# Optimization experiments

Hardware: AMD Instinct MI355X
Metric: run time of the kernel (lower is better)

## Reference

```python
import jax, jax.numpy as jnp
import numpy as np

ATTN_SPLITS = 2
TEMPERATURE = 10000.0

# ---------- split / merge helpers (faithful to split_feature / merge_splits) ----------

def split_cf(x, ns):  # channel-first [b,c,h,w] -> [b*ns*ns, c, h/ns, w/ns]
    b, c, h, w = x.shape
    x = x.reshape(b, c, ns, h // ns, ns, w // ns).transpose(0, 2, 4, 1, 3, 5)
    return x.reshape(b * ns * ns, c, h // ns, w // ns)

def merge_cf(x, ns):  # channel-first inverse
    b, c, h, w = x.shape
    nb = b // (ns * ns)
    x = x.reshape(nb, ns, ns, c, h, w).transpose(0, 3, 1, 4, 2, 5)
    return x.reshape(nb, c, ns * h, ns * w)

def split_cl(x, ns):  # channel-last [b,h,w,c] -> [b*ns*ns, h/ns, w/ns, c]
    b, h, w, c = x.shape
    x = x.reshape(b, ns, h // ns, ns, w // ns, c).transpose(0, 1, 3, 2, 4, 5)
    return x.reshape(b * ns * ns, h // ns, w // ns, c)

def merge_cl(x, ns):  # channel-last inverse
    b, h, w, c = x.shape
    nb = b // (ns * ns)
    x = x.reshape(nb, ns, ns, h, w, c).transpose(0, 1, 3, 2, 4, 5)
    return x.reshape(nb, ns * h, ns * w, c)

# ---------- PositionEmbeddingSine (normalize=True, scale=2*pi) ----------

def pos_embed_sine(h, w, num_pos_feats):
    scale = 2.0 * np.pi
    eps = 1e-6
    ones = jnp.ones((h, w), jnp.float32)
    y_embed = jnp.cumsum(ones, 0)
    x_embed = jnp.cumsum(ones, 1)
    y_embed = y_embed / (y_embed[-1:, :] + eps) * scale
    x_embed = x_embed / (x_embed[:, -1:] + eps) * scale
    dim_t = jnp.arange(num_pos_feats, dtype=jnp.float32)
    dim_t = TEMPERATURE ** (2.0 * jnp.floor(dim_t / 2.0) / num_pos_feats)
    pos_x = x_embed[:, :, None] / dim_t  # [h,w,npf]
    pos_y = y_embed[:, :, None] / dim_t
    pos_x = jnp.stack([jnp.sin(pos_x[:, :, 0::2]), jnp.cos(pos_x[:, :, 1::2])], -1).reshape(h, w, -1)
    pos_y = jnp.stack([jnp.sin(pos_y[:, :, 0::2]), jnp.cos(pos_y[:, :, 1::2])], -1).reshape(h, w, -1)
    pos = jnp.concatenate([pos_y, pos_x], -1)  # [h,w,c]
    return jnp.transpose(pos, (2, 0, 1))[None]  # [1,c,h,w]

def feature_add_position(f0, f1, attn_splits, c):
    if attn_splits > 1:
        f0s = split_cf(f0, attn_splits)
        f1s = split_cf(f1, attn_splits)
        pos = pos_embed_sine(f0s.shape[2], f0s.shape[3], c // 2)
        return merge_cf(f0s + pos, attn_splits), merge_cf(f1s + pos, attn_splits)
    pos = pos_embed_sine(f0.shape[2], f0.shape[3], c // 2)
    return f0 + pos, f1 + pos

# ---------- shifted-window attention mask (static, numpy) ----------

def shift_window_attn_mask(h, w, ns):
    wsh, wsw = h // ns, w // ns
    ssh, ssw = wsh // 2, wsw // 2
    img = np.zeros((h, w), np.float32)
    cnt = 0
    for hs in (slice(0, -wsh), slice(-wsh, -ssh), slice(-ssh, None)):
        for ws in (slice(0, -wsw), slice(-wsw, -ssw), slice(-ssw, None)):
            img[hs, ws] = cnt
            cnt += 1
    m = img.reshape(ns, wsh, ns, wsw).transpose(0, 2, 1, 3).reshape(ns * ns, wsh * wsw)
    am = m[:, None, :] - m[:, :, None]
    am = np.where(am != 0, -100.0, 0.0).astype(np.float32)
    return jnp.asarray(am)  # [ns*ns, N, N]

# ---------- single-head split (shifted) window attention ----------

def split_window_attention(q, k, v, ns, h, w, attn_mask):
    b, _, c = q.shape
    bn = b * ns * ns
    wsh, wsw = h // ns, w // ns
    ssh, ssw = wsh // 2, wsw // 2
    q = q.reshape(b, h, w, c)
    k = k.reshape(b, h, w, c)
    v = v.reshape(b, h, w, c)
    q = jnp.roll(q, (-ssh, -ssw), (1, 2))
    k = jnp.roll(k, (-ssh, -ssw), (1, 2))
    v = jnp.roll(v, (-ssh, -ssw), (1, 2))
    qs = split_cl(q, ns).reshape(bn, -1, c)
    ks = split_cl(k, ns).reshape(bn, -1, c)
    vs = split_cl(v, ns).reshape(bn, -1, c)
    scores = jnp.einsum('bnc,bmc->bnm', qs, ks) / jnp.sqrt(jnp.asarray(c, qs.dtype))
    scores = scores + jnp.tile(attn_mask, (b, 1, 1))
    attn = jax.nn.softmax(scores, axis=-1)
    out = jnp.einsum('bnm,bmc->bnc', attn, vs)
    out = merge_cl(out.reshape(bn, wsh, wsw, c), ns)
    out = jnp.roll(out, (ssh, ssw), (1, 2))
    return out.reshape(b, -1, c)

# ---------- global correlation softmax matching ----------

def global_correlation_softmax(f0, f1):
    b, c, h, w = f0.shape
    f0v = f0.reshape(b, c, -1)  # [b,c,hw]
    f1v = f1.reshape(b, c, -1)
    corr = jnp.einsum('bcn,bcm->bnm', f0v, f1v) / jnp.sqrt(jnp.asarray(c, f0.dtype))
    yy, xx = jnp.meshgrid(jnp.arange(h), jnp.arange(w), indexing='ij')
    grid = jnp.stack([xx, yy], 0).astype(f0.dtype)  # [2,h,w] (x,y)
    gridv = grid.reshape(2, -1).T  # [hw,2]
    prob = jax.nn.softmax(corr, axis=-1)
    corresp = jnp.einsum('bnm,md->bnd', prob, gridv).reshape(b, h, w, 2).transpose(0, 3, 1, 2)
    flow = corresp - grid[None]
    return flow

# ---------- setup & reference ----------

def setup_inputs() -> dict:
    key = jax.random.key(0)
    k0, k1 = jax.random.split(key)
    b, c, h, w = 4, 128, 64, 64
    feature0 = jax.random.normal(k0, (b, c, h, w), jnp.float32)
    feature1 = jax.random.normal(k1, (b, c, h, w), jnp.float32)
    return {'feature0': feature0, 'feature1': feature1}

def reference(feature0, feature1):
    b, c, h, w = feature0.shape
    ns = ATTN_SPLITS
    f0, f1 = feature_add_position(feature0, feature1, ns, c)
    attn_mask = shift_window_attn_mask(h, w, ns)
    q = f0.reshape(b, c, -1).transpose(0, 2, 1)  # [b,hw,c]
    kv = f1.reshape(b, c, -1).transpose(0, 2, 1)
    f0_attn = split_window_attention(q, kv, kv, ns, h, w, attn_mask)  # [b,hw,c]
    f0_attn = f0_attn.transpose(0, 2, 1).reshape(b, c, h, w)
    flow = global_correlation_softmax(f0_attn, f1)  # [b,2,h,w]
    return flow
```

## Files before the change

kernel.cpp:

```cpp
#include <hip/hip_runtime.h>
#include <hip/hip_bf16.h>
#include <math.h>

#define NB 4
#define NC 128
#define NH 64
#define NW 64
#define NHW 4096
#define SCALE 0.08838834764831845f

typedef short bf16x8 __attribute__((ext_vector_type(8)));
typedef float f32x4 __attribute__((ext_vector_type(4)));

__device__ __forceinline__ unsigned bfbits(float f) {
    unsigned u = __float_as_uint(f);
    return (u + 0x7FFFu + ((u >> 16) & 1u)) >> 16;
}
__device__ __forceinline__ unsigned bfpair(float a, float b) {
    return bfbits(a) | (bfbits(b) << 16);
}

__global__ __launch_bounds__(256) void pos_kernel(float* __restrict__ pos) {
    int idx = blockIdx.x * 256 + threadIdx.x;
    if (idx >= NC * 32 * 32) return;
    int x = idx & 31;
    int y = (idx >> 5) & 31;
    int c = idx >> 10;
    const float twopi = 6.283185307179586f;
    const float denom = 32.0f + 1e-6f;
    int cc = (c < 64) ? c : (c - 64);
    float e = (c < 64) ? (float)(y + 1) : (float)(x + 1);
    e = e * (twopi / denom);
    int k = cc >> 1;
    float arg = e * exp2f(-0.41524101186091903f * (float)k);
    pos[idx] = (cc & 1) ? cosf(arg) : sinf(arg);
}

__global__ __launch_bounds__(256) void pack_kernel(
        const float* __restrict__ f0, const float* __restrict__ f1,
        const float* __restrict__ pos,
        __hip_bfloat16* __restrict__ F0t, __hip_bfloat16* __restrict__ Bt,
        __hip_bfloat16* __restrict__ Ktw) {
    __shared__ float T[64][129];
    int blk = blockIdx.x;
    const bool isA = blk < 256;
    const float* src = isA ? f0 : f1;
    blk &= 255;
    const int y = blk & 63;
    const int b = blk >> 6;
    const int tid = threadIdx.x;
    const float* s = src + (size_t)b * NC * NHW + y * 64;
    const float sA = isA ? SCALE : 1.0f;
    for (int idx = tid; idx < 64 * NC; idx += 256) {
        const int x = idx & 63, c = idx >> 6;
        T[x][c] = (s[c * NHW + x] + pos[(c << 10) + ((y & 31) << 5) + (x & 31)]) * sA;
    }
    __syncthreads();
    __hip_bfloat16* dst = isA ? F0t : Bt;
    for (int idx = tid; idx < 512; idx += 256) {
        const int x = idx >> 3, c0 = (idx & 7) * 16;
        const float* tr = &T[x][c0];
        uint4 v0, v1;
        v0.x = bfpair(tr[0], tr[1]);   v0.y = bfpair(tr[2], tr[3]);
        v0.z = bfpair(tr[4], tr[5]);   v0.w = bfpair(tr[6], tr[7]);
        v1.x = bfpair(tr[8], tr[9]);   v1.y = bfpair(tr[10], tr[11]);
        v1.z = bfpair(tr[12], tr[13]); v1.w = bfpair(tr[14], tr[15]);
        __hip_bfloat16* row = dst + ((size_t)b * NHW + y * 64 + x) * NC + c0;
        *reinterpret_cast<uint4*>(row) = v0;
        *reinterpret_cast<uint4*>(row + 8) = v1;
    }
    if (!isA) {
        const int yp = (y + 48) & 63;
        const int wi = yp >> 5, ry = yp & 31;
        const int c = tid >> 1;
        const int wj = tid & 1;
        const int win = b * 4 + wi * 2 + wj;
        unsigned up[16];
        #pragma unroll
        for (int pr = 0; pr < 16; ++pr) {
            const int x0 = ((wj << 5) + 2 * pr + 16) & 63;
            up[pr] = bfpair(T[x0][c], T[x0 + 1][c]);
        }
        __hip_bfloat16* krow = Ktw + ((size_t)win * NC + c) * 1024 + ry * 32;
        uint4* uv = reinterpret_cast<uint4*>(up);
        #pragma unroll
        for (int i = 0; i < 4; ++i)
            *reinterpret_cast<uint4*>(krow + i * 8) = uv[i];
    }
}

__global__ __launch_bounds__(256) void attn_mfma_kernel(
        const __hip_bfloat16* __restrict__ F0t,
        const __hip_bfloat16* __restrict__ Bt,
        const __hip_bfloat16* __restrict__ Ktw,
        __hip_bfloat16* __restrict__ At) {
    __shared__ __align__(16) char lds[73728];
    char* KsB = lds;
    char* VsB = lds + 32768;
    char* Pscr = lds + 65536;
    const int tid = threadIdx.x;
    const int lane = tid & 63;
    const int w = tid >> 6;
    const int l15 = lane & 15;
    const int g = lane >> 4;
    const int blk = blockIdx.x;
    const int win = blk >> 4;
    const int qt = blk & 15;
    const int b = win >> 2, wi = (win >> 1) & 1, wj = win & 1;

    const char* Btb = (const char*)(Bt + (size_t)b * NHW * NC);
    const char* Vsrc = (const char*)(Ktw + (size_t)win * NC * 1024);

    bf16x8 qf[4];
    {
        const int tok = qt * 64 + w * 16 + l15;
        const int yo = ((wi << 5) + (tok >> 5) + 16) & 63;
        const int xo = ((wj << 5) + (tok & 31) + 16) & 63;
        const __hip_bfloat16* qrow =
            F0t + ((size_t)b * NHW + yo * 64 + xo) * NC + g * 8;
        #pragma unroll
        for (int kk = 0; kk < 4; ++kk)
            qf[kk] = *reinterpret_cast<const bf16x8*>(qrow + kk * 32);
    }

    const int reg_q = (wi ? (qt < 8 ? 1 : 2) : 0) * 3
                    + (wj ? ((w & 1) == 0 ? 1 : 2) : 0);

    auto stageK = [&](int buf, int kt) {
        char* dst = KsB + buf * 16384;
        #pragma unroll
        for (int it = 0; it < 4; ++it) {
            const int obase = w * 4096 + it * 1024;
            const int row = w * 16 + it * 4 + (lane >> 4);
            const int tok = kt * 64 + row;
            const int yo = ((wi << 5) + (tok >> 5) + 16) & 63;
            const int xo = ((wj << 5) + (tok & 31) + 16) & 63;
            const char* src = Btb + (yo * 64 + xo) * 256 +
                              (((lane & 15) * 16) ^ ((row & 7) << 4));
            __builtin_amdgcn_global_load_lds(
                (const __attribute__((address_space(1))) void*)src,
                (__attribute__((address_space(3))) void*)(dst + obase), 16, 0, 0);
        }
    };
    auto stageV = [&](int buf, int kt) {
        char* dst = VsB + buf * 16384;
        #pragma unroll
        for (int it = 0; it < 4; ++it) {
            const int obase = w * 4096 + it * 1024;
            const int o = obase + lane * 16;
            const int crow = o >> 7;
            const int off = o & 127;
            __builtin_amdgcn_global_load_lds(
                (const __attribute__((address_space(1))) void*)(Vsrc + crow * 2048 + kt * 128 + (off ^ ((crow & 7) << 4))),
                (__attribute__((address_space(3))) void*)(dst + obase), 16, 0, 0);
        }
    };

    f32x4 oacc[8] = {{0,0,0,0},{0,0,0,0},{0,0,0,0},{0,0,0,0},
                     {0,0,0,0},{0,0,0,0},{0,0,0,0},{0,0,0,0}};
    float zacc = 0.f;

    stageK(0, 0); stageV(0, 0);
    __syncthreads();

    for (int kt = 0; kt < 16; ++kt) {
        const int buf = kt & 1;
        if (kt < 15) { stageK(buf ^ 1, kt + 1); stageV(buf ^ 1, kt + 1); }

        const char* kb = KsB + buf * 16384;
        f32x4 sacc[4] = {{0,0,0,0},{0,0,0,0},{0,0,0,0},{0,0,0,0}};
        #pragma unroll
        for (int kk = 0; kk < 4; ++kk) {
            #pragma unroll
            for (int msub = 0; msub < 4; ++msub) {
                const int byte = msub * 4096 + l15 * 256 + ((kk * 64 + g * 16) ^ ((l15 & 7) << 4));
                bf16x8 kf = *reinterpret_cast<const bf16x8*>(kb + byte);
                sacc[msub] = __builtin_amdgcn_mfma_f32_16x16x32_bf16(kf, qf[kk], sacc[msub], 0, 0, 0);
            }
        }

        const int rk_row = (wi ? (kt < 8 ? 1 : 2) : 0) * 3;
        char* pw = Pscr + w * 2048;
        #pragma unroll
        for (int msub = 0; msub < 4; ++msub) {
            const int rk = rk_row + (wj ? ((msub & 1) == 0 ? 1 : 2) : 0);
            const bool ok = (rk == reg_q);
            const float p0 = ok ? __expf(sacc[msub][0]) : 0.f;
            const float p1 = ok ? __expf(sacc[msub][1]) : 0.f;
            const float p2 = ok ? __expf(sacc[msub][2]) : 0.f;
            const float p3 = ok ? __expf(sacc[msub][3]) : 0.f;
            zacc += (p0 + p1) + (p2 + p3);
            *reinterpret_cast<unsigned*>(pw + l15 * 128 + ((msub * 32 + g * 8 + 0) ^ ((l15 & 7) << 4))) = bfpair(p0, p1);
            *reinterpret_cast<unsigned*>(pw + l15 * 128 + ((msub * 32 + g * 8 + 4) ^ ((l15 & 7) << 4))) = bfpair(p2, p3);
        }
        bf16x8 pf[2];
        #pragma unroll
        for (int kk = 0; kk < 2; ++kk)
            pf[kk] = *reinterpret_cast<const bf16x8*>(pw + l15 * 128 + ((kk * 64 + g * 16) ^ ((l15 & 7) << 4)));

        const char* vb = VsB + buf * 16384;
        #pragma unroll
        for (int kk = 0; kk < 2; ++kk) {
            #pragma unroll
            for (int co = 0; co < 8; ++co) {
                const int byte = (co * 16 + l15) * 128 + ((kk * 64 + g * 16) ^ ((l15 & 7) << 4));
                bf16x8 vf = *reinterpret_cast<const bf16x8*>(vb + byte);
                oacc[co] = __builtin_amdgcn_mfma_f32_16x16x32_bf16(pf[kk], vf, oacc[co], 0, 0, 0);
            }
        }
        __syncthreads();
    }

    float z = zacc;
    z += __shfl_xor(z, 16);
    z += __shfl_xor(z, 32);

    unsigned short* olds = reinterpret_cast<unsigned short*>(lds + w * 4096);
    #pragma unroll
    for (int r = 0; r < 4; ++r) {
        const float zi = SCALE / __shfl(z, g * 4 + r);
        #pragma unroll
        for (int co = 0; co < 8; ++co)
            olds[(g * 4 + r) * 128 + co * 16 + l15] = (unsigned short)bfbits(oacc[co][r] * zi);
    }

    const int qloc = lane >> 2;
    const int c0 = (lane & 3) * 32;
    const int tok = qt * 64 + w * 16 + qloc;
    const int yo = ((wi << 5) + (tok >> 5) + 16) & 63;
    const int xo = ((wj << 5) + (tok & 31) + 16) & 63;
    __hip_bfloat16* arow = At + ((size_t)b * NHW + yo * 64 + xo) * NC + c0;
    #pragma unroll
    for (int i = 0; i < 4; ++i) {
        int4 v = *reinterpret_cast<const int4*>(olds + qloc * 128 + c0 + i * 8);
        *reinterpret_cast<int4*>(arow + i * 8) = v;
    }
}

__global__ __launch_bounds__(256, 2) void corr_part_kernel(
        const __hip_bfloat16* __restrict__ At,
        const __hip_bfloat16* __restrict__ Bt,
        float4* __restrict__ part) {
    __shared__ __hip_bfloat16 Bs[2][64 * 128];
    const int tid = threadIdx.x;
    const int lane = tid & 63;
    const int w = tid >> 6;
    const int blk = blockIdx.x;
    const int ms = blk & 7;
    const int nt = (blk >> 3) & 15;
    const int b = blk >> 7;
    const int l15 = lane & 15;
    const int g = lane >> 4;
    const int n0 = nt * 256 + w * 64;

    const __hip_bfloat16* Ab = At + (size_t)b * NHW * NC;
    const __hip_bfloat16* Bb = Bt + (size_t)b * NHW * NC;

    bf16x8 afrag[4][4];
    #pragma unroll
    for (int s = 0; s < 4; ++s) {
        const __hip_bfloat16* arow = Ab + (size_t)(n0 + s * 16 + l15) * NC + g * 8;
        #pragma unroll
        for (int kk = 0; kk < 4; ++kk)
            afrag[s][kk] = *reinterpret_cast<const bf16x8*>(arow + kk * 32);
    }

    auto stage = [&](int buf, int mtile) {
        const char* srcbase = reinterpret_cast<const char*>(Bb + (size_t)mtile * 64 * NC);
        #pragma unroll
        for (int it = 0; it < 4; ++it) {
            const int obase = w * 4096 + it * 1024;
            const int o = obase + lane * 16;
            const int row = o >> 8;
            const int off = o & 255;
            const char* src = srcbase + row * 256 + (off ^ ((row & 7) << 4));
            __builtin_amdgcn_global_load_lds(
                (const __attribute__((address_space(1))) void*)src,
                (__attribute__((address_space(3))) void*)((char*)&Bs[buf][0] + obase),
                16, 0, 0);
        }
    };

    f32x4 rl[4]  = {{0,0,0,0},{0,0,0,0},{0,0,0,0},{0,0,0,0}};
    f32x4 rsm[4] = {{0,0,0,0},{0,0,0,0},{0,0,0,0},{0,0,0,0}};
    f32x4 rsy[4] = {{0,0,0,0},{0,0,0,0},{0,0,0,0},{0,0,0,0}};

    stage(0, ms * 8);
    __syncthreads();

    for (int mt = 0; mt < 8; ++mt) {
        const int buf = mt & 1;
        if (mt < 7) stage(buf ^ 1, ms * 8 + mt + 1);

        f32x4 acc[4][4] = {{{0,0,0,0},{0,0,0,0},{0,0,0,0},{0,0,0,0}},
                           {{0,0,0,0},{0,0,0,0},{0,0,0,0},{0,0,0,0}},
                           {{0,0,0,0},{0,0,0,0},{0,0,0,0},{0,0,0,0}},
                           {{0,0,0,0},{0,0,0,0},{0,0,0,0},{0,0,0,0}}};
        const char* base = (const char*)&Bs[buf][0];
        #pragma unroll
        for (int kk = 0; kk < 4; ++kk) {
            #pragma unroll
            for (int msub = 0; msub < 4; ++msub) {
                const int byte = msub * 4096 + l15 * 256 +
                                 ((kk * 64 + g * 16) ^ ((l15 & 7) << 4));
                bf16x8 bfrag = *reinterpret_cast<const bf16x8*>(base + byte);
                #pragma unroll
                for (int s = 0; s < 4; ++s)
                    acc[s][msub] = __builtin_amdgcn_mfma_f32_16x16x32_bf16(
                        afrag[s][kk], bfrag, acc[s][msub], 0, 0, 0);
            }
        }
        const float y0 = (float)(ms * 8 + mt);
        #pragma unroll
        for (int s = 0; s < 4; ++s) {
            #pragma unroll
            for (int r = 0; r < 4; ++r) {
                float p0 = __expf(acc[s][0][r]);
                float p1 = __expf(acc[s][1][r]);
                float p2 = __expf(acc[s][2][r]);
                float p3 = __expf(acc[s][3][r]);
                float ts = (p0 + p1) + (p2 + p3);
                rl[s][r]  += ts;
                rsy[s][r] += y0 * ts;
                rsm[s][r] += fmaf(3.f, p3, fmaf(2.f, p2, p1));
            }
        }
        __syncthreads();
    }

    const float xl = (float)l15;
    #pragma unroll
    for (int s = 0; s < 4; ++s) {
        #pragma unroll
        for (int r = 0; r < 4; ++r) {
            float a  = rl[s][r];
            float sx = xl * rl[s][r] + 16.f * rsm[s][r];
            float sy = rsy[s][r];
            #pragma unroll
            for (int m = 1; m < 16; m <<= 1) {
                a  += __shfl_xor(a, m);
                sx += __shfl_xor(sx, m);
                sy += __shfl_xor(sy, m);
            }
            if (l15 == 0) {
                const int n = n0 + s * 16 + g * 4 + r;
                part[((size_t)b * NHW + n) * 8 + ms] = make_float4(a, sx, sy, 0.f);
            }
        }
    }
}

__global__ __launch_bounds__(256) void finalize_kernel(
        const float4* __restrict__ part, float* __restrict__ out) {
    const int idx = blockIdx.x * 256 + threadIdx.x;
    if (idx >= NB * NHW) return;
    const int n = idx & (NHW - 1);
    const int b = idx >> 12;
    float l = 0.f, sx = 0.f, sy = 0.f;
    #pragma unroll
    for (int i = 0; i < 8; ++i) {
        float4 p = part[(size_t)idx * 8 + i];
        l += p.x; sx += p.y; sy += p.z;
    }
    const float inv = 1.0f / l;
    out[(size_t)b * 2 * NHW + n]       = sx * inv - (float)(n & 63);
    out[(size_t)b * 2 * NHW + NHW + n] = sy * inv - (float)(n >> 6);
}

extern "C" void kernel_launch(void* const* d_in, const int* in_sizes, int n_in,
                              void* d_out, int out_size, void* d_ws, size_t ws_size,
                              hipStream_t stream) {
    const float* f0 = (const float*)d_in[0];
    const float* f1 = (const float*)d_in[1];
    float* pos = (float*)d_ws;
    __hip_bfloat16* F0t = (__hip_bfloat16*)(pos + 131072);
    __hip_bfloat16* Bt  = F0t + (size_t)NB * NHW * NC;
    __hip_bfloat16* Ktw = Bt  + (size_t)NB * NHW * NC;
    __hip_bfloat16* At  = Ktw + (size_t)16 * NC * 1024;
    float4* part = (float4*)(At + (size_t)NB * NHW * NC);
    float* out = (float*)d_out;

    pos_kernel<<<512, 256, 0, stream>>>(pos);
    pack_kernel<<<512, 256, 0, stream>>>(f0, f1, pos, F0t, Bt, Ktw);
    attn_mfma_kernel<<<256, 256, 0, stream>>>(F0t, Bt, Ktw, At);
    corr_part_kernel<<<512, 256, 0, stream>>>(At, Bt, part);
    finalize_kernel<<<64, 256, 0, stream>>>(part, out);
}
```

Measured before the change: 70.96 us.

## Split attention key range across wave pairs and read V directly from global

The attention kernel now runs 512 blocks of 32 queries instead of 256 blocks of 64. Wave pairs split the key tiles into even and odd halves and merge their partial outputs and normalizers through LDS at the end. V is no longer staged in LDS and is read straight from global memory. The query scale now folds in log2(e), so both attention and correlation use exp2f, and the attention output is rescaled by the same factor. The kernel also adds launch_bounds occupancy 2, aiming for more parallelism on 256 CUs, at the cost of uncached-in-LDS V reads and an extra reduction step.

```diff
diff --git a/kernel.cpp b/kernel.cpp
--- a/kernel.cpp
+++ b/kernel.cpp
@@ -8,6 +8,7 @@
 #define NW 64
 #define NHW 4096
 #define SCALE 0.08838834764831845f
+#define PSL2E 0.12753102543365835f
 
 typedef short bf16x8 __attribute__((ext_vector_type(8)));
 typedef float f32x4 __attribute__((ext_vector_type(4)));
@@ -50,7 +51,7 @@
     const int b = blk >> 6;
     const int tid = threadIdx.x;
     const float* s = src + (size_t)b * NC * NHW + y * 64;
-    const float sA = isA ? SCALE : 1.0f;
+    const float sA = isA ? PSL2E : 1.0f;
     for (int idx = tid; idx < 64 * NC; idx += 256) {
         const int x = idx & 63, c = idx >> 6;
         T[x][c] = (s[c * NHW + x] + pos[(c << 10) + ((y & 31) << 5) + (x & 31)]) * sA;
@@ -89,23 +90,23 @@
     }
 }
 
-__global__ __launch_bounds__(256) void attn_mfma_kernel(
+__global__ __launch_bounds__(256, 2) void attn_mfma_kernel(
         const __hip_bfloat16* __restrict__ F0t,
         const __hip_bfloat16* __restrict__ Bt,
         const __hip_bfloat16* __restrict__ Ktw,
         __hip_bfloat16* __restrict__ At) {
     __shared__ __align__(16) char lds[73728];
-    char* KsB = lds;
-    char* VsB = lds + 32768;
     char* Pscr = lds + 65536;
     const int tid = threadIdx.x;
     const int lane = tid & 63;
     const int w = tid >> 6;
+    const int p = w & 1;
+    const int qh = w >> 1;
     const int l15 = lane & 15;
     const int g = lane >> 4;
     const int blk = blockIdx.x;
-    const int win = blk >> 4;
-    const int qt = blk & 15;
+    const int win = blk >> 5;
+    const int qt32 = blk & 31;
     const int b = win >> 2, wi = (win >> 1) & 1, wj = win & 1;
 
     const char* Btb = (const char*)(Bt + (size_t)b * NHW * NC);
@@ -113,7 +114,7 @@
 
     bf16x8 qf[4];
     {
-        const int tok = qt * 64 + w * 16 + l15;
+        const int tok = qt32 * 32 + qh * 16 + l15;
         const int yo = ((wi << 5) + (tok >> 5) + 16) & 63;
         const int xo = ((wj << 5) + (tok & 31) + 16) & 63;
         const __hip_bfloat16* qrow =
@@ -123,16 +124,16 @@
             qf[kk] = *reinterpret_cast<const bf16x8*>(qrow + kk * 32);
     }
 
-    const int reg_q = (wi ? (qt < 8 ? 1 : 2) : 0) * 3
-                    + (wj ? ((w & 1) == 0 ? 1 : 2) : 0);
-
-    auto stageK = [&](int buf, int kt) {
-        char* dst = KsB + buf * 16384;
+    const int reg_q = (wi ? (qt32 < 16 ? 1 : 2) : 0) * 3
+                    + (wj ? (qh == 0 ? 1 : 2) : 0);
+
+    auto stageK = [&](int slot, int ktg) {
+        char* dst = lds + slot * 16384;
         #pragma unroll
         for (int it = 0; it < 4; ++it) {
             const int obase = w * 4096 + it * 1024;
             const int row = w * 16 + it * 4 + (lane >> 4);
-            const int tok = kt * 64 + row;
+            const int tok = ktg * 64 + row;
             const int yo = ((wi << 5) + (tok >> 5) + 16) & 63;
             const int xo = ((wj << 5) + (tok & 31) + 16) & 63;
             const char* src = Btb + (yo * 64 + xo) * 256 +
@@ -142,32 +143,20 @@
                 (__attribute__((address_space(3))) void*)(dst + obase), 16, 0, 0);
         }
     };
-    auto stageV = [&](int buf, int kt) {
-        char* dst = VsB + buf * 16384;
-        #pragma unroll
-        for (int it = 0; it < 4; ++it) {
-            const int obase = w * 4096 + it * 1024;
-            const int o = obase + lane * 16;
-            const int crow = o >> 7;
-            const int off = o & 127;
-            __builtin_amdgcn_global_load_lds(
-                (const __attribute__((address_space(1))) void*)(Vsrc + crow * 2048 + kt * 128 + (off ^ ((crow & 7) << 4))),
-                (__attribute__((address_space(3))) void*)(dst + obase), 16, 0, 0);
-        }
-    };
 
     f32x4 oacc[8] = {{0,0,0,0},{0,0,0,0},{0,0,0,0},{0,0,0,0},
                      {0,0,0,0},{0,0,0,0},{0,0,0,0},{0,0,0,0}};
     float zacc = 0.f;
 
-    stageK(0, 0); stageV(0, 0);
+    stageK(0, 0); stageK(1, 1);
     __syncthreads();
 
-    for (int kt = 0; kt < 16; ++kt) {
-        const int buf = kt & 1;
-        if (kt < 15) { stageK(buf ^ 1, kt + 1); stageV(buf ^ 1, kt + 1); }
-
-        const char* kb = KsB + buf * 16384;
+    int d = 0;
+    for (int s = 0; s < 8; ++s) {
+        const int ktg = 2 * s + p;
+        if (s < 7) { stageK((d ^ 1) * 2 + 0, 2 * s + 2); stageK((d ^ 1) * 2 + 1, 2 * s + 3); }
+
+        const char* kb = lds + (d * 2 + p) * 16384;
         f32x4 sacc[4] = {{0,0,0,0},{0,0,0,0},{0,0,0,0},{0,0,0,0}};
         #pragma unroll
         for (int kk = 0; kk < 4; ++kk) {
@@ -179,16 +168,16 @@
             }
         }
 
-        const int rk_row = (wi ? (kt < 8 ? 1 : 2) : 0) * 3;
+        const int rk_row = (wi ? (ktg < 8 ? 1 : 2) : 0) * 3;
         char* pw = Pscr + w * 2048;
         #pragma unroll
         for (int msub = 0; msub < 4; ++msub) {
             const int rk = rk_row + (wj ? ((msub & 1) == 0 ? 1 : 2) : 0);
             const bool ok = (rk == reg_q);
-            const float p0 = ok ? __expf(sacc[msub][0]) : 0.f;
-            const float p1 = ok ? __expf(sacc[msub][1]) : 0.f;
-            const float p2 = ok ? __expf(sacc[msub][2]) : 0.f;
-            const float p3 = ok ? __expf(sacc[msub][3]) : 0.f;
+            const float p0 = ok ? exp2f(sacc[msub][0]) : 0.f;
+            const float p1 = ok ? exp2f(sacc[msub][1]) : 0.f;
+            const float p2 = ok ? exp2f(sacc[msub][2]) : 0.f;
+            const float p3 = ok ? exp2f(sacc[msub][3]) : 0.f;
             zacc += (p0 + p1) + (p2 + p3);
             *reinterpret_cast<unsigned*>(pw + l15 * 128 + ((msub * 32 + g * 8 + 0) ^ ((l15 & 7) << 4))) = bfpair(p0, p1);
             *reinterpret_cast<unsigned*>(pw + l15 * 128 + ((msub * 32 + g * 8 + 4) ^ ((l15 & 7) << 4))) = bfpair(p2, p3);
@@ -198,42 +187,61 @@
         for (int kk = 0; kk < 2; ++kk)
             pf[kk] = *reinterpret_cast<const bf16x8*>(pw + l15 * 128 + ((kk * 64 + g * 16) ^ ((l15 & 7) << 4)));
 
-        const char* vb = VsB + buf * 16384;
-        #pragma unroll
-        for (int kk = 0; kk < 2; ++kk) {
+        #pragma unroll
+        for (int kk2 = 0; kk2 < 2; ++kk2) {
+            const int tok0 = ktg * 64 + kk2 * 32 + g * 8;
             #pragma unroll
             for (int co = 0; co < 8; ++co) {
-                const int byte = (co * 16 + l15) * 128 + ((kk * 64 + g * 16) ^ ((l15 & 7) << 4));
-                bf16x8 vf = *reinterpret_cast<const bf16x8*>(vb + byte);
-                oacc[co] = __builtin_amdgcn_mfma_f32_16x16x32_bf16(pf[kk], vf, oacc[co], 0, 0, 0);
+                const int c = co * 16 + l15;
+                bf16x8 vf = *reinterpret_cast<const bf16x8*>(
+                    Vsrc + ((size_t)c * 1024 + tok0) * 2);
+                oacc[co] = __builtin_amdgcn_mfma_f32_16x16x32_bf16(pf[kk2], vf, oacc[co], 0, 0, 0);
             }
         }
         __syncthreads();
+        d ^= 1;
     }
 
     float z = zacc;
     z += __shfl_xor(z, 16);
     z += __shfl_xor(z, 32);
 
-    unsigned short* olds = reinterpret_cast<unsigned short*>(lds + w * 4096);
-    #pragma unroll
-    for (int r = 0; r < 4; ++r) {
-        const float zi = SCALE / __shfl(z, g * 4 + r);
-        #pragma unroll
-        for (int co = 0; co < 8; ++co)
-            olds[(g * 4 + r) * 128 + co * 16 + l15] = (unsigned short)bfbits(oacc[co][r] * zi);
-    }
-
-    const int qloc = lane >> 2;
-    const int c0 = (lane & 3) * 32;
-    const int tok = qt * 64 + w * 16 + qloc;
-    const int yo = ((wi << 5) + (tok >> 5) + 16) & 63;
-    const int xo = ((wj << 5) + (tok & 31) + 16) & 63;
-    __hip_bfloat16* arow = At + ((size_t)b * NHW + yo * 64 + xo) * NC + c0;
-    #pragma unroll
-    for (int i = 0; i < 4; ++i) {
-        int4 v = *reinterpret_cast<const int4*>(olds + qloc * 128 + c0 + i * 8);
-        *reinterpret_cast<int4*>(arow + i * 8) = v;
+    float* zl = (float*)(lds + 16384);
+    if (p == 1) {
+        float* od = (float*)(lds + qh * 8192);
+        #pragma unroll
+        for (int r = 0; r < 4; ++r) {
+            #pragma unroll
+            for (int co = 0; co < 8; ++co)
+                od[(g * 4 + r) * 128 + co * 16 + l15] = oacc[co][r];
+        }
+        if (lane < 16) zl[qh * 16 + lane] = z;
+    }
+    __syncthreads();
+    if (p == 0) {
+        const float* od = (const float*)(lds + qh * 8192);
+        const float zc = z + zl[qh * 16 + l15];
+        unsigned short* olds = (unsigned short*)(lds + 16896 + qh * 4096);
+        #pragma unroll
+        for (int r = 0; r < 4; ++r) {
+            const float zi = PSL2E / __shfl(zc, g * 4 + r);
+            #pragma unroll
+            for (int co = 0; co < 8; ++co) {
+                const float o = oacc[co][r] + od[(g * 4 + r) * 128 + co * 16 + l15];
+                olds[(g * 4 + r) * 128 + co * 16 + l15] = (unsigned short)bfbits(o * zi);
+            }
+        }
+        const int qloc = lane >> 2;
+        const int c0 = (lane & 3) * 32;
+        const int tok = qt32 * 32 + qh * 16 + qloc;
+        const int yo = ((wi << 5) + (tok >> 5) + 16) & 63;
+        const int xo = ((wj << 5) + (tok & 31) + 16) & 63;
+        __hip_bfloat16* arow = At + ((size_t)b * NHW + yo * 64 + xo) * NC + c0;
+        #pragma unroll
+        for (int i = 0; i < 4; ++i) {
+            int4 v = *reinterpret_cast<const int4*>(olds + qloc * 128 + c0 + i * 8);
+            *reinterpret_cast<int4*>(arow + i * 8) = v;
+        }
     }
 }
 
@@ -315,10 +323,10 @@
         for (int s = 0; s < 4; ++s) {
             #pragma unroll
             for (int r = 0; r < 4; ++r) {
-                float p0 = __expf(acc[s][0][r]);
-                float p1 = __expf(acc[s][1][r]);
-                float p2 = __expf(acc[s][2][r]);
-                float p3 = __expf(acc[s][3][r]);
+                float p0 = exp2f(acc[s][0][r]);
+                float p1 = exp2f(acc[s][1][r]);
+                float p2 = exp2f(acc[s][2][r]);
+                float p3 = exp2f(acc[s][3][r]);
                 float ts = (p0 + p1) + (p2 + p3);
                 rl[s][r]  += ts;
                 rsy[s][r] += y0 * ts;
@@ -382,7 +390,7 @@
 
     pos_kernel<<<512, 256, 0, stream>>>(pos);
     pack_kernel<<<512, 256, 0, stream>>>(f0, f1, pos, F0t, Bt, Ktw);
-    attn_mfma_kernel<<<256, 256, 0, stream>>>(F0t, Bt, Ktw, At);
+    attn_mfma_kernel<<<512, 256, 0, stream>>>(F0t, Bt, Ktw, At);
     corr_part_kernel<<<512, 256, 0, stream>>>(At, Bt, part);
     finalize_kernel<<<64, 256, 0, stream>>>(part, out);
 }
```

Result: slower. 99.28 us (+39.9%).

## Fold log2e into the scale for exp2f, and retile the correlation kernel finer

Applied to the files above, without the earlier changes.

The attention scale is multiplied by log2(e) in the packed queries and in the attention output normalisation. Both softmax stages can then call exp2f directly instead of __expf, which drops a multiply per exponential. The correlation-partial kernel is retiled: each block now covers 128 query rows and 4 key tiles instead of 256 and 8. That takes the grid from 512 to 2048 blocks and drops the two-blocks-per-CU launch bound, to raise parallelism and reduce register pressure. In exchange, each B tile is re-staged by more blocks, and the partial buffer and the finalize reduction double to 16 slices, which assumes the workspace has room for them.

```diff
diff --git a/kernel.cpp b/kernel.cpp
--- a/kernel.cpp
+++ b/kernel.cpp
@@ -8,6 +8,7 @@
 #define NW 64
 #define NHW 4096
 #define SCALE 0.08838834764831845f
+#define PSL2E 0.12753102543365835f
 
 typedef short bf16x8 __attribute__((ext_vector_type(8)));
 typedef float f32x4 __attribute__((ext_vector_type(4)));
@@ -50,7 +51,7 @@
     const int b = blk >> 6;
     const int tid = threadIdx.x;
     const float* s = src + (size_t)b * NC * NHW + y * 64;
-    const float sA = isA ? SCALE : 1.0f;
+    const float sA = isA ? PSL2E : 1.0f;
     for (int idx = tid; idx < 64 * NC; idx += 256) {
         const int x = idx & 63, c = idx >> 6;
         T[x][c] = (s[c * NHW + x] + pos[(c << 10) + ((y & 31) << 5) + (x & 31)]) * sA;
@@ -185,10 +186,10 @@
         for (int msub = 0; msub < 4; ++msub) {
             const int rk = rk_row + (wj ? ((msub & 1) == 0 ? 1 : 2) : 0);
             const bool ok = (rk == reg_q);
-            const float p0 = ok ? __expf(sacc[msub][0]) : 0.f;
-            const float p1 = ok ? __expf(sacc[msub][1]) : 0.f;
-            const float p2 = ok ? __expf(sacc[msub][2]) : 0.f;
-            const float p3 = ok ? __expf(sacc[msub][3]) : 0.f;
+            const float p0 = ok ? exp2f(sacc[msub][0]) : 0.f;
+            const float p1 = ok ? exp2f(sacc[msub][1]) : 0.f;
+            const float p2 = ok ? exp2f(sacc[msub][2]) : 0.f;
+            const float p3 = ok ? exp2f(sacc[msub][3]) : 0.f;
             zacc += (p0 + p1) + (p2 + p3);
             *reinterpret_cast<unsigned*>(pw + l15 * 128 + ((msub * 32 + g * 8 + 0) ^ ((l15 & 7) << 4))) = bfpair(p0, p1);
             *reinterpret_cast<unsigned*>(pw + l15 * 128 + ((msub * 32 + g * 8 + 4) ^ ((l15 & 7) << 4))) = bfpair(p2, p3);
@@ -218,7 +219,7 @@
     unsigned short* olds = reinterpret_cast<unsigned short*>(lds + w * 4096);
     #pragma unroll
     for (int r = 0; r < 4; ++r) {
-        const float zi = SCALE / __shfl(z, g * 4 + r);
+        const float zi = PSL2E / __shfl(z, g * 4 + r);
         #pragma unroll
         for (int co = 0; co < 8; ++co)
             olds[(g * 4 + r) * 128 + co * 16 + l15] = (unsigned short)bfbits(oacc[co][r] * zi);
@@ -237,7 +238,7 @@
     }
 }
 
-__global__ __launch_bounds__(256, 2) void corr_part_kernel(
+__global__ __launch_bounds__(256) void corr_part_kernel(
         const __hip_bfloat16* __restrict__ At,
         const __hip_bfloat16* __restrict__ Bt,
         float4* __restrict__ part) {
@@ -246,19 +247,19 @@
     const int lane = tid & 63;
     const int w = tid >> 6;
     const int blk = blockIdx.x;
-    const int ms = blk & 7;
-    const int nt = (blk >> 3) & 15;
-    const int b = blk >> 7;
+    const int ms = blk & 15;
+    const int nt = (blk >> 4) & 31;
+    const int b = blk >> 9;
     const int l15 = lane & 15;
     const int g = lane >> 4;
-    const int n0 = nt * 256 + w * 64;
+    const int n0 = nt * 128 + w * 32;
 
     const __hip_bfloat16* Ab = At + (size_t)b * NHW * NC;
     const __hip_bfloat16* Bb = Bt + (size_t)b * NHW * NC;
 
-    bf16x8 afrag[4][4];
-    #pragma unroll
-    for (int s = 0; s < 4; ++s) {
+    bf16x8 afrag[2][4];
+    #pragma unroll
+    for (int s = 0; s < 2; ++s) {
         const __hip_bfloat16* arow = Ab + (size_t)(n0 + s * 16 + l15) * NC + g * 8;
         #pragma unroll
         for (int kk = 0; kk < 4; ++kk)
@@ -281,20 +282,18 @@
         }
     };
 
-    f32x4 rl[4]  = {{0,0,0,0},{0,0,0,0},{0,0,0,0},{0,0,0,0}};
-    f32x4 rsm[4] = {{0,0,0,0},{0,0,0,0},{0,0,0,0},{0,0,0,0}};
-    f32x4 rsy[4] = {{0,0,0,0},{0,0,0,0},{0,0,0,0},{0,0,0,0}};
-
-    stage(0, ms * 8);
+    f32x4 rl[2]  = {{0,0,0,0},{0,0,0,0}};
+    f32x4 rsm[2] = {{0,0,0,0},{0,0,0,0}};
+    f32x4 rsy[2] = {{0,0,0,0},{0,0,0,0}};
+
+    stage(0, ms * 4);
     __syncthreads();
 
-    for (int mt = 0; mt < 8; ++mt) {
+    for (int mt = 0; mt < 4; ++mt) {
         const int buf = mt & 1;
-        if (mt < 7) stage(buf ^ 1, ms * 8 + mt + 1);
-
-        f32x4 acc[4][4] = {{{0,0,0,0},{0,0,0,0},{0,0,0,0},{0,0,0,0}},
-                           {{0,0,0,0},{0,0,0,0},{0,0,0,0},{0,0,0,0}},
-                           {{0,0,0,0},{0,0,0,0},{0,0,0,0},{0,0,0,0}},
+        if (mt < 3) stage(buf ^ 1, ms * 4 + mt + 1);
+
+        f32x4 acc[2][4] = {{{0,0,0,0},{0,0,0,0},{0,0,0,0},{0,0,0,0}},
                            {{0,0,0,0},{0,0,0,0},{0,0,0,0},{0,0,0,0}}};
         const char* base = (const char*)&Bs[buf][0];
         #pragma unroll
@@ -304,21 +303,21 @@
                 const int byte = msub * 4096 + l15 * 256 +
                                  ((kk * 64 + g * 16) ^ ((l15 & 7) << 4));
                 bf16x8 bfrag = *reinterpret_cast<const bf16x8*>(base + byte);
-                #pragma unroll
-                for (int s = 0; s < 4; ++s)
-                    acc[s][msub] = __builtin_amdgcn_mfma_f32_16x16x32_bf16(
-                        afrag[s][kk], bfrag, acc[s][msub], 0, 0, 0);
-            }
-        }
-        const float y0 = (float)(ms * 8 + mt);
-        #pragma unroll
-        for (int s = 0; s < 4; ++s) {
+                acc[0][msub] = __builtin_amdgcn_mfma_f32_16x16x32_bf16(
+                    afrag[0][kk], bfrag, acc[0][msub], 0, 0, 0);
+                acc[1][msub] = __builtin_amdgcn_mfma_f32_16x16x32_bf16(
+                    afrag[1][kk], bfrag, acc[1][msub], 0, 0, 0);
+            }
+        }
+        const float y0 = (float)(ms * 4 + mt);
+        #pragma unroll
+        for (int s = 0; s < 2; ++s) {
             #pragma unroll
             for (int r = 0; r < 4; ++r) {
-                float p0 = __expf(acc[s][0][r]);
-                float p1 = __expf(acc[s][1][r]);
-                float p2 = __expf(acc[s][2][r]);
-                float p3 = __expf(acc[s][3][r]);
+                float p0 = exp2f(acc[s][0][r]);
+                float p1 = exp2f(acc[s][1][r]);
+                float p2 = exp2f(acc[s][2][r]);
+                float p3 = exp2f(acc[s][3][r]);
                 float ts = (p0 + p1) + (p2 + p3);
                 rl[s][r]  += ts;
                 rsy[s][r] += y0 * ts;
@@ -330,7 +329,7 @@
 
     const float xl = (float)l15;
     #pragma unroll
-    for (int s = 0; s < 4; ++s) {
+    for (int s = 0; s < 2; ++s) {
         #pragma unroll
         for (int r = 0; r < 4; ++r) {
             float a  = rl[s][r];
@@ -344,7 +343,7 @@
             }
             if (l15 == 0) {
                 const int n = n0 + s * 16 + g * 4 + r;
-                part[((size_t)b * NHW + n) * 8 + ms] = make_float4(a, sx, sy, 0.f);
+                part[((size_t)b * NHW + n) * 16 + ms] = make_float4(a, sx, sy, 0.f);
             }
         }
     }
@@ -358,8 +357,8 @@
     const int b = idx >> 12;
     float l = 0.f, sx = 0.f, sy = 0.f;
     #pragma unroll
-    for (int i = 0; i < 8; ++i) {
-        float4 p = part[(size_t)idx * 8 + i];
+    for (int i = 0; i < 16; ++i) {
+        float4 p = part[(size_t)idx * 16 + i];
         l += p.x; sx += p.y; sy += p.z;
     }
     const float inv = 1.0f / l;
@@ -383,6 +382,6 @@
     pos_kernel<<<512, 256, 0, stream>>>(pos);
     pack_kernel<<<512, 256, 0, stream>>>(f0, f1, pos, F0t, Bt, Ktw);
     attn_mfma_kernel<<<256, 256, 0, stream>>>(F0t, Bt, Ktw, At);
-    corr_part_kernel<<<512, 256, 0, stream>>>(At, Bt, part);
+    corr_part_kernel<<<2048, 256, 0, stream>>>(At, Bt, part);
     finalize_kernel<<<64, 256, 0, stream>>>(part, out);
 }
```

Result: slower. 82.38 us (+16.1%).
